# Kernel tuning notes

Measured on AMD Instinct MI355X. Metric: run time of the kernel, lower is better.

The kernel has to match this reference:

```python
import jax, jax.numpy as jnp
import numpy as np

N, STATE_DIM, HID, D_EMB, K = 8192, 512, 128, 128, 10
EPS = 0.001


def setup_inputs() -> dict:
    key = jax.random.key(0)
    ks = jax.random.split(key, 5)
    sc = lambda fan_in: 1.0 / np.sqrt(fan_in)
    return {
        "s": jax.random.normal(ks[0], (N, STATE_DIM), dtype=jnp.float32),
        "W1": jax.random.normal(ks[1], (HID, STATE_DIM), dtype=jnp.float32) * sc(STATE_DIM),
        "b1": jax.random.normal(ks[2], (HID,), dtype=jnp.float32) * sc(STATE_DIM),
        "W2": jax.random.normal(ks[3], (D_EMB, HID), dtype=jnp.float32) * sc(HID),
        "b2": jax.random.normal(ks[4], (D_EMB,), dtype=jnp.float32) * sc(HID),
        "k": K,
    }


def reference(s, W1, b1, W2, b2, k):
    # embedding: relu(Linear) -> Linear
    x = jax.nn.relu(s @ W1.T + b1) @ W2.T + b2            # [N, d_emb]
    # pairwise L2 distance matrix: ||xi||^2 + ||xj||^2 - 2 xi.xj
    sq = jnp.sum(x * x, axis=1)                            # [N]
    dist2 = sq[:, None] + sq[None, :] - 2.0 * (x @ x.T)    # [N, N]
    # clamp tiny negative values from cancellation (torch.sqrt would NaN)
    dist = jnp.sqrt(jnp.maximum(dist2, 1e-12))             # [N, N]
    # k nearest per row, excluding self (smallest entry = own distance ~0)
    neg_vals, _ = jax.lax.top_k(-dist, k + 1)              # [N, k+1], ascending dist
    k_nearest = -neg_vals[:, 1:]                           # [N, k]
    sum_k_nearest = jnp.sum(k_nearest, axis=1, keepdims=True)  # [N, 1]
    mean_k_nearest_2 = jnp.mean(sum_k_nearest) ** 2
    return EPS / (sum_k_nearest ** 2 / mean_k_nearest_2 + EPS)
```

## Files before the change

### kernel.cpp

```cpp
#include <hip/hip_runtime.h>
#include <hip/hip_bf16.h>

#define NN 8192
#define SD 512
#define HID 128
#define DE 128
#define KP1 11
#define EPSF 0.001f
#define NSPLIT 32
#define NCHUNK NSPLIT
#define CB (NN / NSPLIT)
#define NSUB (CB / 16)
#define PBLK (8 * 2 * KP1 * 16)

using short8 = __attribute__((ext_vector_type(8))) short;
using f32x4 = __attribute__((ext_vector_type(4))) float;

__device__ inline ushort f2bf(float f) {
    __hip_bfloat16 b = __float2bfloat16(f);
    return *reinterpret_cast<ushort*>(&b);
}
__device__ inline float bf2f(ushort u) {
    unsigned v = (unsigned)u << 16;
    union { unsigned u; float f; } c; c.u = v; return c.f;
}

__global__ __launch_bounds__(256) void wsplit_kernel(
    const float* __restrict__ W1, const float* __restrict__ W2,
    ushort* __restrict__ W1h, ushort* __restrict__ W1l,
    ushort* __restrict__ W2h, ushort* __restrict__ W2l)
{
    const int bid = blockIdx.x;
    const float* src; ushort *dh, *dl; int base;
    if (bid < 64) { src = W1; dh = W1h; dl = W1l; base = bid * 1024; }
    else          { src = W2; dh = W2h; dl = W2l; base = (bid - 64) * 1024; }
    const int i = base + threadIdx.x * 4;
    float4 f = *reinterpret_cast<const float4*>(src + i);
    ushort h[4], lo[4];
    float fv[4] = {f.x, f.y, f.z, f.w};
#pragma unroll
    for (int j = 0; j < 4; ++j) {
        h[j] = f2bf(fv[j]);
        lo[j] = f2bf(fv[j] - bf2f(h[j]));
    }
    *reinterpret_cast<uint2*>(dh + i) = *reinterpret_cast<uint2*>(h);
    *reinterpret_cast<uint2*>(dl + i) = *reinterpret_cast<uint2*>(lo);
}

__global__ __launch_bounds__(256) void mlp_kernel(
    const float* __restrict__ s, const ushort* __restrict__ W1h,
    const ushort* __restrict__ W1l, const float* __restrict__ b1,
    const ushort* __restrict__ W2h, const ushort* __restrict__ W2l,
    const float* __restrict__ b2, __hip_bfloat16* __restrict__ xb,
    float* __restrict__ sqb)
{
    __shared__ __align__(16) ushort sbh[2][32 * 32];
    __shared__ __align__(16) ushort sbl[2][32 * 32];
    __shared__ __align__(16) ushort hbh[32 * 128];
    __shared__ __align__(16) ushort hbl[32 * 128];
    __shared__ __align__(16) ushort xtile[32 * 128];
    __shared__ float sqpart[4 * 32];

    const int t = threadIdx.x;
    const int w = t >> 6, l = t & 63;
    const int lc = l & 15, c4 = l >> 4;
    const int rb = blockIdx.x * 32;
    const int cb = w * 32;

    const int srow = t >> 3, skq = t & 7;
    const int ssl = ((skq >> 1) + (srow >> 2)) & 3;
    const int sByte = srow * 64 + (ssl ^ (srow & 3)) * 16 + (skq & 1) * 8;
    const float* sgbase = s + (size_t)(rb + srow) * SD + skq * 4;

    float4 sf;
#define STAGE_LOAD_S(kt_) sf = *reinterpret_cast<const float4*>(sgbase + (kt_) * 32)
#define STAGE_WRITE_S(b_) do { \
    float fv_[4] = {sf.x, sf.y, sf.z, sf.w}; \
    ushort h_[4], lo_[4]; \
    _Pragma("unroll") \
    for (int j_ = 0; j_ < 4; ++j_) { \
        h_[j_] = f2bf(fv_[j_]); \
        lo_[j_] = f2bf(fv_[j_] - bf2f(h_[j_])); \
    } \
    *reinterpret_cast<uint2*>(reinterpret_cast<char*>(sbh[b_]) + sByte) = *reinterpret_cast<uint2*>(h_); \
    *reinterpret_cast<uint2*>(reinterpret_cast<char*>(sbl[b_]) + sByte) = *reinterpret_cast<uint2*>(lo_); \
} while (0)

    int aByte[2];
#pragma unroll
    for (int rt = 0; rt < 2; ++rt) {
        int row = rt * 16 + lc;
        int sl = ((c4 + (row >> 2)) & 3) ^ (row & 3);
        aByte[rt] = row * 64 + sl * 16;
    }

    const ushort* w1hp[2]; const ushort* w1lp[2];
#pragma unroll
    for (int ct = 0; ct < 2; ++ct) {
        int col = cb + ct * 16 + lc;
        w1hp[ct] = W1h + (size_t)col * SD + c4 * 8;
        w1lp[ct] = W1l + (size_t)col * SD + c4 * 8;
    }

    f32x4 acc1[2][2];
#pragma unroll
    for (int rt = 0; rt < 2; ++rt)
#pragma unroll
        for (int ct = 0; ct < 2; ++ct) acc1[rt][ct] = {0.f, 0.f, 0.f, 0.f};

    STAGE_LOAD_S(0);
    STAGE_WRITE_S(0);
    short8 bh[2], bl[2], nbh[2], nbl[2];
#pragma unroll
    for (int ct = 0; ct < 2; ++ct) {
        bh[ct] = *reinterpret_cast<const short8*>(w1hp[ct]);
        bl[ct] = *reinterpret_cast<const short8*>(w1lp[ct]);
    }

    for (int kt = 0; kt < 16; ++kt) {
        __syncthreads();
        if (kt < 15) STAGE_LOAD_S(kt + 1);
        short8 ah[2], al[2];
#pragma unroll
        for (int rt = 0; rt < 2; ++rt) {
            ah[rt] = *reinterpret_cast<const short8*>(
                reinterpret_cast<char*>(sbh[kt & 1]) + aByte[rt]);
            al[rt] = *reinterpret_cast<const short8*>(
                reinterpret_cast<char*>(sbl[kt & 1]) + aByte[rt]);
        }
        if (kt < 15) {
#pragma unroll
            for (int ct = 0; ct < 2; ++ct) {
                nbh[ct] = *reinterpret_cast<const short8*>(w1hp[ct] + (kt + 1) * 32);
                nbl[ct] = *reinterpret_cast<const short8*>(w1lp[ct] + (kt + 1) * 32);
            }
        }
#pragma unroll
        for (int rt = 0; rt < 2; ++rt)
#pragma unroll
            for (int ct = 0; ct < 2; ++ct) {
                acc1[rt][ct] = __builtin_amdgcn_mfma_f32_16x16x32_bf16(ah[rt], bh[ct], acc1[rt][ct], 0, 0, 0);
                acc1[rt][ct] = __builtin_amdgcn_mfma_f32_16x16x32_bf16(ah[rt], bl[ct], acc1[rt][ct], 0, 0, 0);
                acc1[rt][ct] = __builtin_amdgcn_mfma_f32_16x16x32_bf16(al[rt], bh[ct], acc1[rt][ct], 0, 0, 0);
            }
        if (kt < 15) {
            STAGE_WRITE_S((kt + 1) & 1);
#pragma unroll
            for (int ct = 0; ct < 2; ++ct) { bh[ct] = nbh[ct]; bl[ct] = nbl[ct]; }
        }
    }

    float b1v[2];
#pragma unroll
    for (int ct = 0; ct < 2; ++ct) b1v[ct] = b1[cb + ct * 16 + lc];
#pragma unroll
    for (int rt = 0; rt < 2; ++rt)
#pragma unroll
        for (int ct = 0; ct < 2; ++ct)
#pragma unroll
            for (int reg = 0; reg < 4; ++reg) {
                float v = fmaxf(acc1[rt][ct][reg] + b1v[ct], 0.f);
                ushort hh = f2bf(v);
                ushort hl = f2bf(v - bf2f(hh));
                int row = rt * 16 + c4 * 4 + reg;
                int kcol = cb + ct * 16 + lc;
                int sl = (kcol >> 3) ^ (row & 15);
                int byte = row * 256 + sl * 16 + (kcol & 7) * 2;
                *reinterpret_cast<ushort*>(reinterpret_cast<char*>(hbh) + byte) = hh;
                *reinterpret_cast<ushort*>(reinterpret_cast<char*>(hbl) + byte) = hl;
            }
    __syncthreads();

    f32x4 acc2[2][2];
#pragma unroll
    for (int rt = 0; rt < 2; ++rt)
#pragma unroll
        for (int ct = 0; ct < 2; ++ct) acc2[rt][ct] = {0.f, 0.f, 0.f, 0.f};

#pragma unroll
    for (int kt = 0; kt < 4; ++kt) {
        short8 ah[2], al[2];
#pragma unroll
        for (int rt = 0; rt < 2; ++rt) {
            int row = rt * 16 + lc;
            int sl = (kt * 4 + c4) ^ (row & 15);
            int byte = row * 256 + sl * 16;
            ah[rt] = *reinterpret_cast<const short8*>(reinterpret_cast<char*>(hbh) + byte);
            al[rt] = *reinterpret_cast<const short8*>(reinterpret_cast<char*>(hbl) + byte);
        }
        short8 wh[2], wl[2];
#pragma unroll
        for (int ct = 0; ct < 2; ++ct) {
            int col = cb + ct * 16 + lc;
            wh[ct] = *reinterpret_cast<const short8*>(W2h + (size_t)col * HID + kt * 32 + c4 * 8);
            wl[ct] = *reinterpret_cast<const short8*>(W2l + (size_t)col * HID + kt * 32 + c4 * 8);
        }
#pragma unroll
        for (int rt = 0; rt < 2; ++rt)
#pragma unroll
            for (int ct = 0; ct < 2; ++ct) {
                acc2[rt][ct] = __builtin_amdgcn_mfma_f32_16x16x32_bf16(ah[rt], wh[ct], acc2[rt][ct], 0, 0, 0);
                acc2[rt][ct] = __builtin_amdgcn_mfma_f32_16x16x32_bf16(ah[rt], wl[ct], acc2[rt][ct], 0, 0, 0);
                acc2[rt][ct] = __builtin_amdgcn_mfma_f32_16x16x32_bf16(al[rt], wh[ct], acc2[rt][ct], 0, 0, 0);
            }
    }

    float b2v[2];
#pragma unroll
    for (int ct = 0; ct < 2; ++ct) b2v[ct] = b2[cb + ct * 16 + lc];
    float p[8];
#pragma unroll
    for (int j = 0; j < 8; ++j) p[j] = 0.f;
#pragma unroll
    for (int rt = 0; rt < 2; ++rt)
#pragma unroll
        for (int ct = 0; ct < 2; ++ct)
#pragma unroll
            for (int reg = 0; reg < 4; ++reg) {
                float v = acc2[rt][ct][reg] + b2v[ct];
                ushort xv = f2bf(v);
                float xf = bf2f(xv);
                p[rt * 4 + reg] = fmaf(xf, xf, p[rt * 4 + reg]);
                int row = rt * 16 + c4 * 4 + reg;
                int e = cb + ct * 16 + lc;
                xtile[row * 128 + e] = xv;
            }
#pragma unroll
    for (int j = 0; j < 8; ++j) {
#pragma unroll
        for (int off = 8; off >= 1; off >>= 1) p[j] += __shfl_xor(p[j], off, 16);
    }
    if (lc == 0) {
#pragma unroll
        for (int rt = 0; rt < 2; ++rt)
#pragma unroll
            for (int reg = 0; reg < 4; ++reg)
                sqpart[w * 32 + rt * 16 + c4 * 4 + reg] = p[rt * 4 + reg];
    }
    __syncthreads();
    if (t < 32)
        sqb[rb + t] = sqpart[t] + sqpart[32 + t] + sqpart[64 + t] + sqpart[96 + t];
    const short8* xsv = reinterpret_cast<const short8*>(xtile);
    short8* xg = reinterpret_cast<short8*>(reinterpret_cast<ushort*>(xb) + (size_t)rb * DE);
    xg[t] = xsv[t];
    xg[t + 256] = xsv[t + 256];
}

__global__ __launch_bounds__(512) void knn_kernel(
    const ushort* __restrict__ xs, const float* __restrict__ sqb,
    float* __restrict__ part)
{
    __shared__ __align__(16) ushort lbuf[CB * DE];
    __shared__ __align__(16) float sqs[CB];

    const int bid = blockIdx.x;
    const int rid = bid >> 5, cid = bid & 31;
    const int t = threadIdx.x;
    const int w = t >> 6, l = t & 63;
    const int q16 = l & 15, lg = l >> 4;
    const int kk = lg * 8;
    const int qb = rid * 256 + w * 32;
    const int cstart = cid * CB;

    {
        const ushort* sb = xs + (size_t)cstart * DE;
#pragma unroll
        for (int i = 0; i < 8; ++i) {
            int sl = t + 512 * i;
            int row = sl >> 4, col = sl & 15;
            short8 v = *reinterpret_cast<const short8*>(sb + row * DE + col * 8);
            *reinterpret_cast<short8*>(&lbuf[(row * 16 + (col ^ (row & 7))) * 8]) = v;
        }
        if (t < 64)
            reinterpret_cast<float4*>(sqs)[t] =
                reinterpret_cast<const float4*>(sqb + cstart)[t];
    }

    short8 bq[2][4];
#pragma unroll
    for (int qs = 0; qs < 2; ++qs)
#pragma unroll
        for (int kb = 0; kb < 4; ++kb)
            bq[qs][kb] = *reinterpret_cast<const short8*>(
                xs + (size_t)(qb + qs * 16 + q16) * DE + kb * 32 + kk);

    float m[2][KP1];
#pragma unroll
    for (int qs = 0; qs < 2; ++qs)
#pragma unroll
        for (int j = 0; j < KP1; ++j) m[qs][j] = 1e30f;

#define INS(qs_, v_) do { \
    float d2_ = (v_); \
    _Pragma("unroll") \
    for (int j_ = KP1 - 1; j_ >= 1; --j_) \
        m[qs_][j_] = __builtin_amdgcn_fmed3f(d2_, m[qs_][j_ - 1], m[qs_][j_]); \
    m[qs_][0] = fminf(d2_, m[qs_][0]); \
} while (0)

    int aIdx[4];
#pragma unroll
    for (int kb = 0; kb < 4; ++kb)
        aIdx[kb] = (q16 * 16 + ((kb * 4 + lg) ^ (q16 & 7))) * 8;

    __syncthreads();

    for (int st = 0; st < NSUB; ++st) {
        const ushort* lb = lbuf + st * 2048;
        short8 fa[4];
#pragma unroll
        for (int kb = 0; kb < 4; ++kb)
            fa[kb] = *reinterpret_cast<const short8*>(lb + aIdx[kb]);
        float4 sv = *reinterpret_cast<const float4*>(sqs + st * 16 + lg * 4);
#pragma unroll
        for (int qs = 0; qs < 2; ++qs) {
            f32x4 acc = {0.f, 0.f, 0.f, 0.f};
#pragma unroll
            for (int kb = 0; kb < 4; ++kb)
                acc = __builtin_amdgcn_mfma_f32_16x16x32_bf16(fa[kb], bq[qs][kb], acc, 0, 0, 0);
            INS(qs, fmaf(-2.f, acc[0], sv.x));
            INS(qs, fmaf(-2.f, acc[1], sv.y));
            INS(qs, fmaf(-2.f, acc[2], sv.z));
            INS(qs, fmaf(-2.f, acc[3], sv.w));
        }
    }

    __syncthreads();
    float* mb = reinterpret_cast<float*>(lbuf);
#pragma unroll
    for (int qs = 0; qs < 2; ++qs)
#pragma unroll
        for (int j = 0; j < KP1; ++j)
            mb[(((w * 2 + qs) * 4 + lg) * KP1 + j) * 16 + q16] = m[qs][j];
    __syncthreads();
    if (l < 32) {
        const int qs = l >> 4, qq = l & 15;
        float mm[KP1];
#pragma unroll
        for (int j = 0; j < KP1; ++j)
            mm[j] = mb[(((w * 2 + qs) * 4 + 0) * KP1 + j) * 16 + qq];
#pragma unroll
        for (int g = 1; g < 4; ++g)
#pragma unroll
            for (int j = 0; j < KP1; ++j) {
                float d2 = mb[(((w * 2 + qs) * 4 + g) * KP1 + j) * 16 + qq];
#pragma unroll
                for (int jj = KP1 - 1; jj >= 1; --jj)
                    mm[jj] = __builtin_amdgcn_fmed3f(d2, mm[jj - 1], mm[jj]);
                mm[0] = fminf(d2, mm[0]);
            }
        float* pout = part + (size_t)bid * PBLK;
#pragma unroll
        for (int j = 0; j < KP1; ++j)
            pout[((w * 2 + qs) * KP1 + j) * 16 + qq] = mm[j];
    }
}

__global__ __launch_bounds__(256) void merge_kernel(
    const float* __restrict__ part, const float* __restrict__ sqb,
    float* __restrict__ sumk, float* __restrict__ psum)
{
    const int row = blockIdx.x * 256 + threadIdx.x;
    const int rid = row >> 8;
    const int sub = ((row >> 5) & 7) * 2 + ((row >> 4) & 1);
    const int lane = row & 15;
    const float* pbase = part + (size_t)rid * NSPLIT * PBLK + sub * (KP1 * 16) + lane;

    float m[KP1];
#pragma unroll
    for (int j = 0; j < KP1; ++j) m[j] = 1e30f;
#pragma unroll 4
    for (int ch = 0; ch < NCHUNK; ++ch) {
        const float* pc = pbase + ch * PBLK;
#pragma unroll
        for (int j = 0; j < KP1; ++j) {
            float d2 = pc[j * 16];
#pragma unroll
            for (int jj = KP1 - 1; jj >= 1; --jj)
                m[jj] = __builtin_amdgcn_fmed3f(d2, m[jj - 1], m[jj]);
            m[0] = fminf(d2, m[0]);
        }
    }
    const float sqq = sqb[row];
    float sum = 0.f;
#pragma unroll
    for (int j = 1; j < KP1; ++j)
        sum += sqrtf(fmaxf(m[j] + sqq, 1e-12f));
    sumk[row] = sum;

    float p = sum;
#pragma unroll
    for (int off = 32; off >= 1; off >>= 1) p += __shfl_xor(p, off, 64);
    __shared__ float red[4];
    if ((threadIdx.x & 63) == 0) red[threadIdx.x >> 6] = p;
    __syncthreads();
    if (threadIdx.x == 0) psum[blockIdx.x] = red[0] + red[1] + red[2] + red[3];
}

__global__ __launch_bounds__(256) void final_kernel(
    const float* __restrict__ sumk, const float* __restrict__ psum,
    float* __restrict__ out)
{
    __shared__ float qsh;
    const int t = threadIdx.x;
    if (t < 64) {
        float p = (t < 32) ? psum[t] : 0.f;
#pragma unroll
        for (int off = 32; off >= 1; off >>= 1) p += __shfl_xor(p, off, 64);
        if (t == 0) {
            float mean = p * (1.0f / NN);
            qsh = EPSF * mean * mean;
        }
    }
    __syncthreads();
    const float qq = qsh;
    const int i = blockIdx.x * 256 + t;
    const float sv = sumk[i];
    out[i] = qq / (fmaf(sv, sv, qq));
}

extern "C" void kernel_launch(void* const* d_in, const int* in_sizes, int n_in,
                              void* d_out, int out_size, void* d_ws, size_t ws_size,
                              hipStream_t stream)
{
    const float* s  = (const float*)d_in[0];
    const float* W1 = (const float*)d_in[1];
    const float* b1 = (const float*)d_in[2];
    const float* W2 = (const float*)d_in[3];
    const float* b2 = (const float*)d_in[4];
    float* out = (float*)d_out;

    char* ws = (char*)d_ws;
    __hip_bfloat16* xb = (__hip_bfloat16*)ws;
    float* sqb  = (float*)(ws + (size_t)NN * DE * 2);
    float* part = sqb + NN;
    float* sumk = part + (size_t)1024 * PBLK;
    float* psum = sumk + NN;
    ushort* W1h = (ushort*)(psum + 32);
    ushort* W1l = W1h + (size_t)HID * SD;
    ushort* W2h = W1l + (size_t)HID * SD;
    ushort* W2l = W2h + (size_t)DE * HID;

    wsplit_kernel<<<80, 256, 0, stream>>>(W1, W2, W1h, W1l, W2h, W2l);
    mlp_kernel<<<NN / 32, 256, 0, stream>>>(s, W1h, W1l, b1, W2h, W2l, b2, xb, sqb);
    knn_kernel<<<(NN / 256) * NSPLIT, 512, 0, stream>>>((const ushort*)xb, sqb, part);
    merge_kernel<<<NN / 256, 256, 0, stream>>>(part, sqb, sumk, psum);
    final_kernel<<<NN / 256, 256, 0, stream>>>(sumk, psum, out);
}
```

Measured before the change: 80.01 us.

## Double MLP block to 8 waves and software-prefetch LDS fragments in knn loop

The MLP kernel now runs 512 threads per block, with each wave owning 16 output columns instead of 32, so per-wave MFMA work and register use shrink and more waves can hide latency. The s staging is reworked to match: each thread loads a float2 and writes 4-byte packed hi/lo halves. Separately, the knn inner loop prefetches the next subtile's A fragments and squared norms from LDS before the current MFMAs, to overlap LDS latency with compute. This costs extra registers in knn, which may lower occupancy.

```diff
diff --git a/kernel.cpp b/kernel.cpp
--- a/kernel.cpp
+++ b/kernel.cpp
@@ -47,7 +47,7 @@
     *reinterpret_cast<uint2*>(dl + i) = *reinterpret_cast<uint2*>(lo);
 }
 
-__global__ __launch_bounds__(256) void mlp_kernel(
+__global__ __launch_bounds__(512) void mlp_kernel(
     const float* __restrict__ s, const ushort* __restrict__ W1h,
     const ushort* __restrict__ W1l, const float* __restrict__ b1,
     const ushort* __restrict__ W2h, const ushort* __restrict__ W2l,
@@ -59,31 +59,28 @@
     __shared__ __align__(16) ushort hbh[32 * 128];
     __shared__ __align__(16) ushort hbl[32 * 128];
     __shared__ __align__(16) ushort xtile[32 * 128];
-    __shared__ float sqpart[4 * 32];
+    __shared__ float sqpart[8 * 32];
 
     const int t = threadIdx.x;
     const int w = t >> 6, l = t & 63;
     const int lc = l & 15, c4 = l >> 4;
     const int rb = blockIdx.x * 32;
-    const int cb = w * 32;
-
-    const int srow = t >> 3, skq = t & 7;
-    const int ssl = ((skq >> 1) + (srow >> 2)) & 3;
-    const int sByte = srow * 64 + (ssl ^ (srow & 3)) * 16 + (skq & 1) * 8;
-    const float* sgbase = s + (size_t)(rb + srow) * SD + skq * 4;
-
-    float4 sf;
-#define STAGE_LOAD_S(kt_) sf = *reinterpret_cast<const float4*>(sgbase + (kt_) * 32)
+    const int cb = w * 16;
+
+    const int srow = t >> 4, sk = t & 15;
+    const int ssl = ((sk >> 2) + (srow >> 2)) & 3;
+    const int sByte = srow * 64 + (ssl ^ (srow & 3)) * 16 + (sk & 3) * 4;
+    const float* sgbase = s + (size_t)(rb + srow) * SD + sk * 2;
+
+    float2 sf;
+#define STAGE_LOAD_S(kt_) sf = *reinterpret_cast<const float2*>(sgbase + (kt_) * 32)
 #define STAGE_WRITE_S(b_) do { \
-    float fv_[4] = {sf.x, sf.y, sf.z, sf.w}; \
-    ushort h_[4], lo_[4]; \
-    _Pragma("unroll") \
-    for (int j_ = 0; j_ < 4; ++j_) { \
-        h_[j_] = f2bf(fv_[j_]); \
-        lo_[j_] = f2bf(fv_[j_] - bf2f(h_[j_])); \
-    } \
-    *reinterpret_cast<uint2*>(reinterpret_cast<char*>(sbh[b_]) + sByte) = *reinterpret_cast<uint2*>(h_); \
-    *reinterpret_cast<uint2*>(reinterpret_cast<char*>(sbl[b_]) + sByte) = *reinterpret_cast<uint2*>(lo_); \
+    ushort h0_ = f2bf(sf.x), h1_ = f2bf(sf.y); \
+    ushort l0_ = f2bf(sf.x - bf2f(h0_)), l1_ = f2bf(sf.y - bf2f(h1_)); \
+    *reinterpret_cast<unsigned*>(reinterpret_cast<char*>(sbh[b_]) + sByte) = \
+        (unsigned)h0_ | ((unsigned)h1_ << 16); \
+    *reinterpret_cast<unsigned*>(reinterpret_cast<char*>(sbl[b_]) + sByte) = \
+        (unsigned)l0_ | ((unsigned)l1_ << 16); \
 } while (0)
 
     int aByte[2];
@@ -94,28 +91,19 @@
         aByte[rt] = row * 64 + sl * 16;
     }
 
-    const ushort* w1hp[2]; const ushort* w1lp[2];
-#pragma unroll
-    for (int ct = 0; ct < 2; ++ct) {
-        int col = cb + ct * 16 + lc;
-        w1hp[ct] = W1h + (size_t)col * SD + c4 * 8;
-        w1lp[ct] = W1l + (size_t)col * SD + c4 * 8;
-    }
-
-    f32x4 acc1[2][2];
-#pragma unroll
-    for (int rt = 0; rt < 2; ++rt)
-#pragma unroll
-        for (int ct = 0; ct < 2; ++ct) acc1[rt][ct] = {0.f, 0.f, 0.f, 0.f};
+    const int col = cb + lc;
+    const ushort* w1hp = W1h + (size_t)col * SD + c4 * 8;
+    const ushort* w1lp = W1l + (size_t)col * SD + c4 * 8;
+
+    f32x4 acc1[2];
+#pragma unroll
+    for (int rt = 0; rt < 2; ++rt) acc1[rt] = {0.f, 0.f, 0.f, 0.f};
 
     STAGE_LOAD_S(0);
     STAGE_WRITE_S(0);
-    short8 bh[2], bl[2], nbh[2], nbl[2];
-#pragma unroll
-    for (int ct = 0; ct < 2; ++ct) {
-        bh[ct] = *reinterpret_cast<const short8*>(w1hp[ct]);
-        bl[ct] = *reinterpret_cast<const short8*>(w1lp[ct]);
-    }
+    short8 bh = *reinterpret_cast<const short8*>(w1hp);
+    short8 bl = *reinterpret_cast<const short8*>(w1lp);
+    short8 nbh, nbl;
 
     for (int kt = 0; kt < 16; ++kt) {
         __syncthreads();
@@ -129,53 +117,40 @@
                 reinterpret_cast<char*>(sbl[kt & 1]) + aByte[rt]);
         }
         if (kt < 15) {
-#pragma unroll
-            for (int ct = 0; ct < 2; ++ct) {
-                nbh[ct] = *reinterpret_cast<const short8*>(w1hp[ct] + (kt + 1) * 32);
-                nbl[ct] = *reinterpret_cast<const short8*>(w1lp[ct] + (kt + 1) * 32);
-            }
-        }
-#pragma unroll
-        for (int rt = 0; rt < 2; ++rt)
-#pragma unroll
-            for (int ct = 0; ct < 2; ++ct) {
-                acc1[rt][ct] = __builtin_amdgcn_mfma_f32_16x16x32_bf16(ah[rt], bh[ct], acc1[rt][ct], 0, 0, 0);
-                acc1[rt][ct] = __builtin_amdgcn_mfma_f32_16x16x32_bf16(ah[rt], bl[ct], acc1[rt][ct], 0, 0, 0);
-                acc1[rt][ct] = __builtin_amdgcn_mfma_f32_16x16x32_bf16(al[rt], bh[ct], acc1[rt][ct], 0, 0, 0);
-            }
+            nbh = *reinterpret_cast<const short8*>(w1hp + (kt + 1) * 32);
+            nbl = *reinterpret_cast<const short8*>(w1lp + (kt + 1) * 32);
+        }
+#pragma unroll
+        for (int rt = 0; rt < 2; ++rt) {
+            acc1[rt] = __builtin_amdgcn_mfma_f32_16x16x32_bf16(ah[rt], bh, acc1[rt], 0, 0, 0);
+            acc1[rt] = __builtin_amdgcn_mfma_f32_16x16x32_bf16(ah[rt], bl, acc1[rt], 0, 0, 0);
+            acc1[rt] = __builtin_amdgcn_mfma_f32_16x16x32_bf16(al[rt], bh, acc1[rt], 0, 0, 0);
+        }
         if (kt < 15) {
             STAGE_WRITE_S((kt + 1) & 1);
-#pragma unroll
-            for (int ct = 0; ct < 2; ++ct) { bh[ct] = nbh[ct]; bl[ct] = nbl[ct]; }
-        }
-    }
-
-    float b1v[2];
-#pragma unroll
-    for (int ct = 0; ct < 2; ++ct) b1v[ct] = b1[cb + ct * 16 + lc];
+            bh = nbh; bl = nbl;
+        }
+    }
+
+    const float b1v = b1[col];
 #pragma unroll
     for (int rt = 0; rt < 2; ++rt)
 #pragma unroll
-        for (int ct = 0; ct < 2; ++ct)
-#pragma unroll
-            for (int reg = 0; reg < 4; ++reg) {
-                float v = fmaxf(acc1[rt][ct][reg] + b1v[ct], 0.f);
-                ushort hh = f2bf(v);
-                ushort hl = f2bf(v - bf2f(hh));
-                int row = rt * 16 + c4 * 4 + reg;
-                int kcol = cb + ct * 16 + lc;
-                int sl = (kcol >> 3) ^ (row & 15);
-                int byte = row * 256 + sl * 16 + (kcol & 7) * 2;
-                *reinterpret_cast<ushort*>(reinterpret_cast<char*>(hbh) + byte) = hh;
-                *reinterpret_cast<ushort*>(reinterpret_cast<char*>(hbl) + byte) = hl;
-            }
-    __syncthreads();
-
-    f32x4 acc2[2][2];
-#pragma unroll
-    for (int rt = 0; rt < 2; ++rt)
-#pragma unroll
-        for (int ct = 0; ct < 2; ++ct) acc2[rt][ct] = {0.f, 0.f, 0.f, 0.f};
+        for (int reg = 0; reg < 4; ++reg) {
+            float v = fmaxf(acc1[rt][reg] + b1v, 0.f);
+            ushort hh = f2bf(v);
+            ushort hl = f2bf(v - bf2f(hh));
+            int row = rt * 16 + c4 * 4 + reg;
+            int sl = (col >> 3) ^ (row & 15);
+            int byte = row * 256 + sl * 16 + (col & 7) * 2;
+            *reinterpret_cast<ushort*>(reinterpret_cast<char*>(hbh) + byte) = hh;
+            *reinterpret_cast<ushort*>(reinterpret_cast<char*>(hbl) + byte) = hl;
+        }
+    __syncthreads();
+
+    f32x4 acc2[2];
+#pragma unroll
+    for (int rt = 0; rt < 2; ++rt) acc2[rt] = {0.f, 0.f, 0.f, 0.f};
 
 #pragma unroll
     for (int kt = 0; kt < 4; ++kt) {
@@ -188,43 +163,31 @@
             ah[rt] = *reinterpret_cast<const short8*>(reinterpret_cast<char*>(hbh) + byte);
             al[rt] = *reinterpret_cast<const short8*>(reinterpret_cast<char*>(hbl) + byte);
         }
-        short8 wh[2], wl[2];
-#pragma unroll
-        for (int ct = 0; ct < 2; ++ct) {
-            int col = cb + ct * 16 + lc;
-            wh[ct] = *reinterpret_cast<const short8*>(W2h + (size_t)col * HID + kt * 32 + c4 * 8);
-            wl[ct] = *reinterpret_cast<const short8*>(W2l + (size_t)col * HID + kt * 32 + c4 * 8);
-        }
-#pragma unroll
-        for (int rt = 0; rt < 2; ++rt)
-#pragma unroll
-            for (int ct = 0; ct < 2; ++ct) {
-                acc2[rt][ct] = __builtin_amdgcn_mfma_f32_16x16x32_bf16(ah[rt], wh[ct], acc2[rt][ct], 0, 0, 0);
-                acc2[rt][ct] = __builtin_amdgcn_mfma_f32_16x16x32_bf16(ah[rt], wl[ct], acc2[rt][ct], 0, 0, 0);
-                acc2[rt][ct] = __builtin_amdgcn_mfma_f32_16x16x32_bf16(al[rt], wh[ct], acc2[rt][ct], 0, 0, 0);
-            }
-    }
-
-    float b2v[2];
-#pragma unroll
-    for (int ct = 0; ct < 2; ++ct) b2v[ct] = b2[cb + ct * 16 + lc];
+        short8 wh = *reinterpret_cast<const short8*>(W2h + (size_t)col * HID + kt * 32 + c4 * 8);
+        short8 wl = *reinterpret_cast<const short8*>(W2l + (size_t)col * HID + kt * 32 + c4 * 8);
+#pragma unroll
+        for (int rt = 0; rt < 2; ++rt) {
+            acc2[rt] = __builtin_amdgcn_mfma_f32_16x16x32_bf16(ah[rt], wh, acc2[rt], 0, 0, 0);
+            acc2[rt] = __builtin_amdgcn_mfma_f32_16x16x32_bf16(ah[rt], wl, acc2[rt], 0, 0, 0);
+            acc2[rt] = __builtin_amdgcn_mfma_f32_16x16x32_bf16(al[rt], wh, acc2[rt], 0, 0, 0);
+        }
+    }
+
+    const float b2v = b2[col];
     float p[8];
 #pragma unroll
     for (int j = 0; j < 8; ++j) p[j] = 0.f;
 #pragma unroll
     for (int rt = 0; rt < 2; ++rt)
 #pragma unroll
-        for (int ct = 0; ct < 2; ++ct)
-#pragma unroll
-            for (int reg = 0; reg < 4; ++reg) {
-                float v = acc2[rt][ct][reg] + b2v[ct];
-                ushort xv = f2bf(v);
-                float xf = bf2f(xv);
-                p[rt * 4 + reg] = fmaf(xf, xf, p[rt * 4 + reg]);
-                int row = rt * 16 + c4 * 4 + reg;
-                int e = cb + ct * 16 + lc;
-                xtile[row * 128 + e] = xv;
-            }
+        for (int reg = 0; reg < 4; ++reg) {
+            float v = acc2[rt][reg] + b2v;
+            ushort xv = f2bf(v);
+            float xf = bf2f(xv);
+            p[rt * 4 + reg] = fmaf(xf, xf, p[rt * 4 + reg]);
+            int row = rt * 16 + c4 * 4 + reg;
+            xtile[row * 128 + col] = xv;
+        }
 #pragma unroll
     for (int j = 0; j < 8; ++j) {
 #pragma unroll
@@ -238,12 +201,15 @@
                 sqpart[w * 32 + rt * 16 + c4 * 4 + reg] = p[rt * 4 + reg];
     }
     __syncthreads();
-    if (t < 32)
-        sqb[rb + t] = sqpart[t] + sqpart[32 + t] + sqpart[64 + t] + sqpart[96 + t];
+    if (t < 32) {
+        float sq = 0.f;
+#pragma unroll
+        for (int ww = 0; ww < 8; ++ww) sq += sqpart[ww * 32 + t];
+        sqb[rb + t] = sq;
+    }
     const short8* xsv = reinterpret_cast<const short8*>(xtile);
     short8* xg = reinterpret_cast<short8*>(reinterpret_cast<ushort*>(xb) + (size_t)rb * DE);
     xg[t] = xsv[t];
-    xg[t + 256] = xsv[t + 256];
 }
 
 __global__ __launch_bounds__(512) void knn_kernel(
@@ -305,13 +271,21 @@
 
     __syncthreads();
 
+    short8 fa[4], fnext[4];
+    float4 sv, svnext;
+#pragma unroll
+    for (int kb = 0; kb < 4; ++kb)
+        fa[kb] = *reinterpret_cast<const short8*>(lbuf + aIdx[kb]);
+    sv = *reinterpret_cast<const float4*>(sqs + lg * 4);
+
     for (int st = 0; st < NSUB; ++st) {
-        const ushort* lb = lbuf + st * 2048;
-        short8 fa[4];
-#pragma unroll
-        for (int kb = 0; kb < 4; ++kb)
-            fa[kb] = *reinterpret_cast<const short8*>(lb + aIdx[kb]);
-        float4 sv = *reinterpret_cast<const float4*>(sqs + st * 16 + lg * 4);
+        if (st + 1 < NSUB) {
+            const ushort* lbn = lbuf + (st + 1) * 2048;
+#pragma unroll
+            for (int kb = 0; kb < 4; ++kb)
+                fnext[kb] = *reinterpret_cast<const short8*>(lbn + aIdx[kb]);
+            svnext = *reinterpret_cast<const float4*>(sqs + (st + 1) * 16 + lg * 4);
+        }
 #pragma unroll
         for (int qs = 0; qs < 2; ++qs) {
             f32x4 acc = {0.f, 0.f, 0.f, 0.f};
@@ -322,6 +296,11 @@
             INS(qs, fmaf(-2.f, acc[1], sv.y));
             INS(qs, fmaf(-2.f, acc[2], sv.z));
             INS(qs, fmaf(-2.f, acc[3], sv.w));
+        }
+        if (st + 1 < NSUB) {
+#pragma unroll
+            for (int kb = 0; kb < 4; ++kb) fa[kb] = fnext[kb];
+            sv = svnext;
         }
     }
 
@@ -442,7 +421,7 @@
     ushort* W2l = W2h + (size_t)DE * HID;
 
     wsplit_kernel<<<80, 256, 0, stream>>>(W1, W2, W1h, W1l, W2h, W2l);
-    mlp_kernel<<<NN / 32, 256, 0, stream>>>(s, W1h, W1l, b1, W2h, W2l, b2, xb, sqb);
+    mlp_kernel<<<NN / 32, 512, 0, stream>>>(s, W1h, W1l, b1, W2h, W2l, b2, xb, sqb);
     knn_kernel<<<(NN / 256) * NSPLIT, 512, 0, stream>>>((const ushort*)xb, sqb, part);
     merge_kernel<<<NN / 256, 256, 0, stream>>>(part, sqb, sumk, psum);
     final_kernel<<<NN / 256, 256, 0, stream>>>(sumk, psum, out);
```

Measured after the change: 81.20 us. No clear change (+1.5%).

## Fold sq/2 and negation into MFMA accumulator, double column splits, shrink LDS merge

Applied to the files above, without the earlier changes.

The kNN kernel now seeds the MFMA accumulator with half the column squared norms and flips the sign bits of the query fragments. The accumulator therefore yields sq_j/2 - xi·xj directly, which removes the per-element fma before the top-k insertion. The column dimension is split 64 ways instead of 32, doubling the block count and halving the LDS tile, which should raise occupancy. The in-block merge is done one query subtile at a time, and the merge kernel rescales by 2 before adding the row norm. In exchange, partial-result traffic and the number of chunks the merge kernel reads both double.

```diff
diff --git a/kernel.cpp b/kernel.cpp
--- a/kernel.cpp
+++ b/kernel.cpp
@@ -7,7 +7,7 @@
 #define DE 128
 #define KP1 11
 #define EPSF 0.001f
-#define NSPLIT 32
+#define NSPLIT 64
 #define NCHUNK NSPLIT
 #define CB (NN / NSPLIT)
 #define NSUB (CB / 16)
@@ -254,7 +254,7 @@
     __shared__ __align__(16) float sqs[CB];
 
     const int bid = blockIdx.x;
-    const int rid = bid >> 5, cid = bid & 31;
+    const int rid = bid >> 6, cid = bid & 63;
     const int t = threadIdx.x;
     const int w = t >> 6, l = t & 63;
     const int q16 = l & 15, lg = l >> 4;
@@ -265,24 +265,30 @@
     {
         const ushort* sb = xs + (size_t)cstart * DE;
 #pragma unroll
-        for (int i = 0; i < 8; ++i) {
+        for (int i = 0; i < 4; ++i) {
             int sl = t + 512 * i;
             int row = sl >> 4, col = sl & 15;
             short8 v = *reinterpret_cast<const short8*>(sb + row * DE + col * 8);
             *reinterpret_cast<short8*>(&lbuf[(row * 16 + (col ^ (row & 7))) * 8]) = v;
         }
-        if (t < 64)
-            reinterpret_cast<float4*>(sqs)[t] =
-                reinterpret_cast<const float4*>(sqb + cstart)[t];
+        if (t < 32) {
+            float4 v = reinterpret_cast<const float4*>(sqb + cstart)[t];
+            v.x *= 0.5f; v.y *= 0.5f; v.z *= 0.5f; v.w *= 0.5f;
+            reinterpret_cast<float4*>(sqs)[t] = v;
+        }
     }
 
     short8 bq[2][4];
 #pragma unroll
     for (int qs = 0; qs < 2; ++qs)
 #pragma unroll
-        for (int kb = 0; kb < 4; ++kb)
+        for (int kb = 0; kb < 4; ++kb) {
             bq[qs][kb] = *reinterpret_cast<const short8*>(
                 xs + (size_t)(qb + qs * 16 + q16) * DE + kb * 32 + kk);
+            unsigned* u = reinterpret_cast<unsigned*>(&bq[qs][kb]);
+#pragma unroll
+            for (int i = 0; i < 4; ++i) u[i] ^= 0x80008000u;
+        }
 
     float m[2][KP1];
 #pragma unroll
@@ -314,45 +320,45 @@
         float4 sv = *reinterpret_cast<const float4*>(sqs + st * 16 + lg * 4);
 #pragma unroll
         for (int qs = 0; qs < 2; ++qs) {
-            f32x4 acc = {0.f, 0.f, 0.f, 0.f};
+            f32x4 acc = {sv.x, sv.y, sv.z, sv.w};
 #pragma unroll
             for (int kb = 0; kb < 4; ++kb)
                 acc = __builtin_amdgcn_mfma_f32_16x16x32_bf16(fa[kb], bq[qs][kb], acc, 0, 0, 0);
-            INS(qs, fmaf(-2.f, acc[0], sv.x));
-            INS(qs, fmaf(-2.f, acc[1], sv.y));
-            INS(qs, fmaf(-2.f, acc[2], sv.z));
-            INS(qs, fmaf(-2.f, acc[3], sv.w));
-        }
-    }
-
-    __syncthreads();
+            INS(qs, acc[0]);
+            INS(qs, acc[1]);
+            INS(qs, acc[2]);
+            INS(qs, acc[3]);
+        }
+    }
+
     float* mb = reinterpret_cast<float*>(lbuf);
-#pragma unroll
-    for (int qs = 0; qs < 2; ++qs)
+    float* pout = part + (size_t)bid * PBLK;
+#pragma unroll
+    for (int qs = 0; qs < 2; ++qs) {
+        __syncthreads();
 #pragma unroll
         for (int j = 0; j < KP1; ++j)
-            mb[(((w * 2 + qs) * 4 + lg) * KP1 + j) * 16 + q16] = m[qs][j];
-    __syncthreads();
-    if (l < 32) {
-        const int qs = l >> 4, qq = l & 15;
-        float mm[KP1];
-#pragma unroll
-        for (int j = 0; j < KP1; ++j)
-            mm[j] = mb[(((w * 2 + qs) * 4 + 0) * KP1 + j) * 16 + qq];
-#pragma unroll
-        for (int g = 1; g < 4; ++g)
-#pragma unroll
-            for (int j = 0; j < KP1; ++j) {
-                float d2 = mb[(((w * 2 + qs) * 4 + g) * KP1 + j) * 16 + qq];
-#pragma unroll
-                for (int jj = KP1 - 1; jj >= 1; --jj)
-                    mm[jj] = __builtin_amdgcn_fmed3f(d2, mm[jj - 1], mm[jj]);
-                mm[0] = fminf(d2, mm[0]);
-            }
-        float* pout = part + (size_t)bid * PBLK;
-#pragma unroll
-        for (int j = 0; j < KP1; ++j)
-            pout[((w * 2 + qs) * KP1 + j) * 16 + qq] = mm[j];
+            mb[((w * 4 + lg) * KP1 + j) * 16 + q16] = m[qs][j];
+        __syncthreads();
+        if (l < 16) {
+            float mm[KP1];
+#pragma unroll
+            for (int j = 0; j < KP1; ++j)
+                mm[j] = mb[((w * 4 + 0) * KP1 + j) * 16 + l];
+#pragma unroll
+            for (int g = 1; g < 4; ++g)
+#pragma unroll
+                for (int j = 0; j < KP1; ++j) {
+                    float d2 = mb[((w * 4 + g) * KP1 + j) * 16 + l];
+#pragma unroll
+                    for (int jj = KP1 - 1; jj >= 1; --jj)
+                        mm[jj] = __builtin_amdgcn_fmed3f(d2, mm[jj - 1], mm[jj]);
+                    mm[0] = fminf(d2, mm[0]);
+                }
+#pragma unroll
+            for (int j = 0; j < KP1; ++j)
+                pout[((w * 2 + qs) * KP1 + j) * 16 + l] = mm[j];
+        }
     }
 }
 
@@ -385,7 +391,7 @@
     float sum = 0.f;
 #pragma unroll
     for (int j = 1; j < KP1; ++j)
-        sum += sqrtf(fmaxf(m[j] + sqq, 1e-12f));
+        sum += sqrtf(fmaxf(fmaf(2.f, m[j], sqq), 1e-12f));
     sumk[row] = sum;
 
     float p = sum;
@@ -434,7 +440,7 @@
     __hip_bfloat16* xb = (__hip_bfloat16*)ws;
     float* sqb  = (float*)(ws + (size_t)NN * DE * 2);
     float* part = sqb + NN;
-    float* sumk = part + (size_t)1024 * PBLK;
+    float* sumk = part + (size_t)2048 * PBLK;
     float* psum = sumk + NN;
     ushort* W1h = (ushort*)(psum + 32);
     ushort* W1l = W1h + (size_t)HID * SD;
```

After: 107.6 us. 34.5% more time.

## Parallelize top-k merge across 32 lanes per row with shuffle butterfly

Applied to the files above, without the earlier changes.

The merge kernel previously had one thread per row serially merging 32 chunk partial top-11 lists, with only 32 blocks launched. Now each row gets 32 lanes: each lane loads one chunk's list, and the lists are combined in a 5-step xor-shuffle butterfly. The grid becomes 1024 blocks, so the final kernel now reduces 1024 partial sums, and the workspace offset is enlarged to match. This trades redundant merge work across lanes and more shuffles for far more parallelism and coalesced-ish loads in a latency-bound tail kernel.

```diff
diff --git a/kernel.cpp b/kernel.cpp
--- a/kernel.cpp
+++ b/kernel.cpp
@@ -360,41 +360,51 @@
     const float* __restrict__ part, const float* __restrict__ sqb,
     float* __restrict__ sumk, float* __restrict__ psum)
 {
-    const int row = blockIdx.x * 256 + threadIdx.x;
+    __shared__ float rowsum[8];
+    const int t = threadIdx.x;
+    const int ww = t >> 6, l = t & 63;
+    const int half = l >> 5, c = l & 31;
+    const int row = blockIdx.x * 8 + ww * 2 + half;
     const int rid = row >> 8;
-    const int sub = ((row >> 5) & 7) * 2 + ((row >> 4) & 1);
-    const int lane = row & 15;
-    const float* pbase = part + (size_t)rid * NSPLIT * PBLK + sub * (KP1 * 16) + lane;
+    const int sub = (row >> 4) & 15;
+    const int qq = row & 15;
+    const float* pl = part + (size_t)(rid * 32 + c) * PBLK + sub * (KP1 * 16) + qq;
 
     float m[KP1];
 #pragma unroll
-    for (int j = 0; j < KP1; ++j) m[j] = 1e30f;
-#pragma unroll 4
-    for (int ch = 0; ch < NCHUNK; ++ch) {
-        const float* pc = pbase + ch * PBLK;
+    for (int j = 0; j < KP1; ++j) m[j] = pl[j * 16];
+
+#pragma unroll
+    for (int s = 1; s <= 16; s <<= 1) {
+        float o[KP1];
+#pragma unroll
+        for (int j = 0; j < KP1; ++j) o[j] = __shfl_xor(m[j], s, 64);
 #pragma unroll
         for (int j = 0; j < KP1; ++j) {
-            float d2 = pc[j * 16];
+            float d2 = o[j];
 #pragma unroll
             for (int jj = KP1 - 1; jj >= 1; --jj)
                 m[jj] = __builtin_amdgcn_fmed3f(d2, m[jj - 1], m[jj]);
             m[0] = fminf(d2, m[0]);
         }
     }
-    const float sqq = sqb[row];
-    float sum = 0.f;
-#pragma unroll
-    for (int j = 1; j < KP1; ++j)
-        sum += sqrtf(fmaxf(m[j] + sqq, 1e-12f));
-    sumk[row] = sum;
-
-    float p = sum;
-#pragma unroll
-    for (int off = 32; off >= 1; off >>= 1) p += __shfl_xor(p, off, 64);
-    __shared__ float red[4];
-    if ((threadIdx.x & 63) == 0) red[threadIdx.x >> 6] = p;
-    __syncthreads();
-    if (threadIdx.x == 0) psum[blockIdx.x] = red[0] + red[1] + red[2] + red[3];
+
+    if (c == 0) {
+        const float sqq = sqb[row];
+        float sum = 0.f;
+#pragma unroll
+        for (int j = 1; j < KP1; ++j)
+            sum += sqrtf(fmaxf(m[j] + sqq, 1e-12f));
+        sumk[row] = sum;
+        rowsum[ww * 2 + half] = sum;
+    }
+    __syncthreads();
+    if (t == 0) {
+        float p = 0.f;
+#pragma unroll
+        for (int i = 0; i < 8; ++i) p += rowsum[i];
+        psum[blockIdx.x] = p;
+    }
 }
 
 __global__ __launch_bounds__(256) void final_kernel(
@@ -402,15 +412,20 @@
     float* __restrict__ out)
 {
     __shared__ float qsh;
+    __shared__ float red[4];
     const int t = threadIdx.x;
-    if (t < 64) {
-        float p = (t < 32) ? psum[t] : 0.f;
+    {
+        float p = 0.f;
+#pragma unroll
+        for (int i = 0; i < 4; ++i) p += psum[t + i * 256];
 #pragma unroll
         for (int off = 32; off >= 1; off >>= 1) p += __shfl_xor(p, off, 64);
-        if (t == 0) {
-            float mean = p * (1.0f / NN);
-            qsh = EPSF * mean * mean;
-        }
+        if ((t & 63) == 0) red[t >> 6] = p;
+    }
+    __syncthreads();
+    if (t == 0) {
+        float mean = (red[0] + red[1] + red[2] + red[3]) * (1.0f / NN);
+        qsh = EPSF * mean * mean;
     }
     __syncthreads();
     const float qq = qsh;
@@ -436,7 +451,7 @@
     float* part = sqb + NN;
     float* sumk = part + (size_t)1024 * PBLK;
     float* psum = sumk + NN;
-    ushort* W1h = (ushort*)(psum + 32);
+    ushort* W1h = (ushort*)(psum + 1024);
     ushort* W1l = W1h + (size_t)HID * SD;
     ushort* W2h = W1l + (size_t)HID * SD;
     ushort* W2l = W2h + (size_t)DE * HID;
@@ -444,6 +459,6 @@
     wsplit_kernel<<<80, 256, 0, stream>>>(W1, W2, W1h, W1l, W2h, W2l);
     mlp_kernel<<<NN / 32, 256, 0, stream>>>(s, W1h, W1l, b1, W2h, W2l, b2, xb, sqb);
     knn_kernel<<<(NN / 256) * NSPLIT, 512, 0, stream>>>((const ushort*)xb, sqb, part);
-    merge_kernel<<<NN / 256, 256, 0, stream>>>(part, sqb, sumk, psum);
+    merge_kernel<<<NN / 8, 256, 0, stream>>>(part, sqb, sumk, psum);
     final_kernel<<<NN / 256, 256, 0, stream>>>(sumk, psum, out);
 }
```

After: 77.07 us. 3.7% less time.
